# Performance work log

Measured on AMD Instinct MI355X. Metric: run time of the kernel, lower is better.

Reference implementation:

```python
import jax, jax.numpy as jnp
import numpy as np
import math

L, Bt, IN, H = 512, 128, 512, 60


def setup_inputs() -> dict:
    key = jax.random.key(0)
    k1, k2, k3 = jax.random.split(key, 3)
    inp = jax.random.normal(k1, (L, Bt, IN), dtype=jnp.float32)
    W = jax.random.normal(k2, (H, IN), dtype=jnp.float32) / np.sqrt(IN)
    b = jnp.zeros((H,), dtype=jnp.float32)
    alphabet = jax.random.uniform(k3, (H, 3), dtype=jnp.float32, minval=-math.pi, maxval=math.pi)
    bond_lengths = jnp.array([132.868, 145.801, 152.326], dtype=jnp.float32)
    bond_angles = jnp.array([2.028, 2.124, 1.941], dtype=jnp.float32)
    return {"inp": inp, "W": W, "b": b, "alphabet": alphabet,
            "bond_lengths": bond_lengths, "bond_angles": bond_angles}


def reference(inp, W, b, alphabet, bond_lengths, bond_angles):
    Lr, Bb = inp.shape[0], inp.shape[1]
    # mixture over alphabet of torsion angles
    x = jax.nn.softmax(inp @ W.T + b, axis=2)                 # (L, B, H)
    phi = jnp.arctan2(x @ jnp.sin(alphabet), x @ jnp.cos(alphabet))  # (L, B, 3)
    # per residue i the loop consumes phi[i].T -> bond index is fastest axis
    phi_f = phi.transpose(0, 2, 1).reshape(Lr * 3, Bb)        # (3L, B)
    r = jnp.tile(bond_lengths, Lr)[:, None]                   # (3L, 1)
    th = jnp.tile(bond_angles, Lr)[:, None]                   # (3L, 1)
    # SRF coordinates of every new atom
    c_tilde = jnp.stack([
        (r * jnp.cos(th)) * jnp.ones_like(phi_f),
        r * jnp.cos(phi_f) * jnp.sin(th),
        r * jnp.sin(phi_f) * jnp.sin(th),
    ], axis=-1)                                               # (3L, B, 3)

    e = jnp.eye(3, dtype=inp.dtype)
    carry0 = (jnp.broadcast_to(e[0], (Bb, 3)),
              jnp.broadcast_to(e[1], (Bb, 3)),
              jnp.broadcast_to(e[2], (Bb, 3)))

    def step(carry, ct):
        A, Bp, C = carry                                      # each (B, 3)
        BC = C - Bp
        bc = BC / jnp.linalg.norm(BC, axis=1, keepdims=True)
        AB = Bp - A
        Nv = jnp.cross(AB, bc)
        n = Nv / jnp.linalg.norm(Nv, axis=1, keepdims=True)
        # D = C + R @ c_tilde, R columns = [bc, n x bc, n]
        D = C + bc * ct[:, 0:1] + jnp.cross(n, bc) * ct[:, 1:2] + n * ct[:, 2:3]
        return (Bp, C, D), D

    _, coords = jax.lax.scan(step, carry0, c_tilde)           # (3L, B, 3)
    return coords
```

## Files before the change

kernel.cpp:

```cpp
#include <hip/hip_runtime.h>
#include <math.h>

#define LSEQ  512
#define BT    128
#define INF   512
#define HH    60
#define NSTEP 1536
#define CH2   6

#define MTILE 64
#define KSTG  128
#define BROW  136

typedef __attribute__((ext_vector_type(8))) short bf16x8;
typedef __attribute__((ext_vector_type(4))) float floatx4;

__device__ __forceinline__ unsigned cvt_pk_bf16(float lo, float hi) {
  unsigned r;
  asm("v_cvt_pk_bf16_f32 %0, %1, %2" : "=v"(r) : "v"(lo), "v"(hi));
  return r;
}
__device__ __forceinline__ void split_pair(float a0, float a1,
                                           unsigned& hw, unsigned& lw) {
  hw = cvt_pk_bf16(a0, a1);
  float h0 = __uint_as_float(hw << 16);
  float h1 = __uint_as_float(hw & 0xFFFF0000u);
  lw = cvt_pk_bf16(a0 - h0, a1 - h1);
}


#define ISSUE_A(BUF, KB) \
  { _Pragma("unroll") \
    for (int ks_ = 0; ks_ < 4; ++ks_) { \
      BUF[2*ks_]   = *(const float4*)(ap0 + (KB) + ks_*32); \
      BUF[2*ks_+1] = *(const float4*)(ap0 + (KB) + ks_*32 + 4); } }

#define STAGE_W(KB) \
  { _Pragma("unroll") \
    for (int i_ = 0; i_ < 8; ++i_) { \
      const int chunk_ = i_ * 256 + tid; \
      const int r_  = chunk_ >> 5; \
      const int j4_ = (chunk_ & 31) * 4; \
      float4 wv_ = make_float4(0.f, 0.f, 0.f, 0.f); \
      if (r_ < HH) wv_ = *(const float4*)(W + (size_t)r_ * INF + (KB) + j4_); \
      unsigned h01_, l01_, h23_, l23_; \
      split_pair(wv_.x, wv_.y, h01_, l01_); \
      split_pair(wv_.z, wv_.w, h23_, l23_); \
      *(uint2*)&BhL[r_ * BROW + j4_] = make_uint2(h01_, h23_); \
      *(uint2*)&BlL[r_ * BROW + j4_] = make_uint2(l01_, l23_); } }

#define DO_STEPS(BUF) \
  { _Pragma("unroll") \
    for (int ks_ = 0; ks_ < 4; ++ks_) { \
      const int kl_ = ks_ * 32; \
      float4 x_ = BUF[2*ks_], y_ = BUF[2*ks_+1]; \
      uint4 uh_, ul_; \
      split_pair(x_.x, x_.y, uh_.x, ul_.x); \
      split_pair(x_.z, x_.w, uh_.y, ul_.y); \
      split_pair(y_.x, y_.y, uh_.z, ul_.z); \
      split_pair(y_.z, y_.w, uh_.w, ul_.w); \
      bf16x8 Ah_ = __builtin_bit_cast(bf16x8, uh_); \
      bf16x8 Al_ = __builtin_bit_cast(bf16x8, ul_); \
      _Pragma("unroll") \
      for (int nt_ = 0; nt_ < 4; ++nt_) { \
        const int boff_ = (nt_ * 16 + c) * BROW + kl_ + quad * 8; \
        bf16x8 Bh_ = *(const bf16x8*)&BhL[boff_]; \
        bf16x8 Bl_ = *(const bf16x8*)&BlL[boff_]; \
        acc[nt_] = __builtin_amdgcn_mfma_f32_16x16x32_bf16(Ah_, Bh_, acc[nt_], 0, 0, 0); \
        acc[nt_] = __builtin_amdgcn_mfma_f32_16x16x32_bf16(Ah_, Bl_, acc[nt_], 0, 0, 0); \
        acc[nt_] = __builtin_amdgcn_mfma_f32_16x16x32_bf16(Al_, Bh_, acc[nt_], 0, 0, 0); } } }

__global__ __launch_bounds__(256, 3) void k_phi(
    const float* __restrict__ inp, const float* __restrict__ W,
    const float* __restrict__ bias, const float* __restrict__ alphabet,
    float* __restrict__ phi_out) {
  __shared__ unsigned short BhL[64 * BROW];
  __shared__ unsigned short BlL[64 * BROW];
  __shared__ float sS[HH * 3], sC[HH * 3], sBias[64];

  const int tid  = threadIdx.x;
  const int lane = tid & 63;
  const int wid  = tid >> 6;
  const int c    = lane & 15;
  const int quad = lane >> 4;
  const int row0 = blockIdx.x * MTILE;

  if (tid < HH * 3) { float a = alphabet[tid]; sS[tid] = __sinf(a); sC[tid] = __cosf(a); }
  if (tid >= 192 && tid < 256) { int n = tid - 192; sBias[n] = (n < HH) ? bias[n] : 0.f; }

  floatx4 acc[4];
#pragma unroll
  for (int nt = 0; nt < 4; ++nt) acc[nt] = (floatx4){0.f, 0.f, 0.f, 0.f};

  const float* ap0 = inp + (size_t)(row0 + wid * 16 + c) * INF + quad * 8;

  float4 A0[8], A1[8];

  ISSUE_A(A0, 0);
  STAGE_W(0);
  __syncthreads();
  ISSUE_A(A1, KSTG);
  DO_STEPS(A0);
  __syncthreads();
  STAGE_W(KSTG);
  __syncthreads();
  ISSUE_A(A0, 2 * KSTG);
  DO_STEPS(A1);
  __syncthreads();
  STAGE_W(2 * KSTG);
  __syncthreads();
  ISSUE_A(A1, 3 * KSTG);
  DO_STEPS(A0);
  __syncthreads();
  STAGE_W(3 * KSTG);
  __syncthreads();
  DO_STEPS(A1);

#pragma unroll
  for (int reg = 0; reg < 4; ++reg) {
    float lg[4];  bool val[4];
#pragma unroll
    for (int nt = 0; nt < 4; ++nt) {
      const int n = nt * 16 + c;
      val[nt] = (n < HH);
      lg[nt] = acc[nt][reg] + sBias[n];
    }
    float m = -1e30f;
#pragma unroll
    for (int nt = 0; nt < 4; ++nt) if (val[nt]) m = fmaxf(m, lg[nt]);
#pragma unroll
    for (int d = 1; d < 16; d <<= 1) m = fmaxf(m, __shfl_xor(m, d, 64));

    float s0=0.f,c0=0.f,s1=0.f,c1=0.f,s2=0.f,c2=0.f;
#pragma unroll
    for (int nt = 0; nt < 4; ++nt) {
      const int n = nt * 16 + c;
      float e = val[nt] ? __expf(lg[nt] - m) : 0.f;
      s0 = fmaf(e, sS[n*3+0], s0);  c0 = fmaf(e, sC[n*3+0], c0);
      s1 = fmaf(e, sS[n*3+1], s1);  c1 = fmaf(e, sC[n*3+1], c1);
      s2 = fmaf(e, sS[n*3+2], s2);  c2 = fmaf(e, sC[n*3+2], c2);
    }
#pragma unroll
    for (int d = 1; d < 16; d <<= 1) {
      s0 += __shfl_xor(s0, d, 64);  c0 += __shfl_xor(c0, d, 64);
      s1 += __shfl_xor(s1, d, 64);  c1 += __shfl_xor(c1, d, 64);
      s2 += __shfl_xor(s2, d, 64);  c2 += __shfl_xor(c2, d, 64);
    }
    if (c == 0) {
      const int row = row0 + wid * 16 + quad * 4 + reg;
      const int l  = row >> 7;
      const int bb = row & 127;
      float* pp = phi_out + (size_t)bb * NSTEP + 3 * l;
      pp[0] = atan2f(s0, c0);
      pp[1] = atan2f(s1, c1);
      pp[2] = atan2f(s2, c2);
    }
  }
}

struct Xf { float r[9]; float p[3]; };

__device__ __forceinline__ Xf compose(const Xf& A, const Xf& B) {
  Xf o;
#pragma unroll
  for (int i = 0; i < 3; ++i) {
#pragma unroll
    for (int j = 0; j < 3; ++j) {
      o.r[i*3+j] = fmaf(A.r[i*3+0], B.r[0+j],
                   fmaf(A.r[i*3+1], B.r[3+j],
                        A.r[i*3+2] * B.r[6+j]));
    }
    o.p[i] = fmaf(A.r[i*3+0], B.p[0],
             fmaf(A.r[i*3+1], B.p[1],
             fmaf(A.r[i*3+2], B.p[2], A.p[i])));
  }
  return o;
}

__device__ __forceinline__ Xf make_T(float phi, float st, float ct, float r) {
  float sp = __sinf(phi), cp = __cosf(phi);
  Xf T;
  T.r[0] = ct;      T.r[1] = -st;     T.r[2] = 0.f;
  T.r[3] = cp * st; T.r[4] = ct * cp; T.r[5] = -sp;
  T.r[6] = sp * st; T.r[7] = ct * sp; T.r[8] = cp;
  T.p[0] = r * ct;  T.p[1] = r * T.r[3]; T.p[2] = r * T.r[6];
  return T;
}

__device__ __forceinline__ void set_identity(Xf& X) {
  X.r[0]=1.f; X.r[1]=0.f; X.r[2]=0.f;
  X.r[3]=0.f; X.r[4]=1.f; X.r[5]=0.f;
  X.r[6]=0.f; X.r[7]=0.f; X.r[8]=1.f;
  X.p[0]=0.f; X.p[1]=0.f; X.p[2]=0.f;
}

__global__ __launch_bounds__(256) void k_scan(
    const float* __restrict__ phi, const float* __restrict__ bl,
    const float* __restrict__ ba, float* __restrict__ out) {
  __shared__ Xf wt[4];

  const int b = blockIdx.x;
  const int t = threadIdx.x & 63;
  const int w = threadIdx.x >> 6;
  const int g = threadIdx.x;

  float st[3], ct[3], rr[3];
#pragma unroll
  for (int j = 0; j < 3; ++j) {
    float a = ba[j];
    st[j] = __sinf(a); ct[j] = __cosf(a); rr[j] = bl[j];
  }

  float f[CH2];
  const float2* ph2 = (const float2*)(phi + (size_t)b * NSTEP + g * CH2);
#pragma unroll
  for (int q = 0; q < CH2/2; ++q) {
    float2 v = ph2[q];
    f[2*q+0] = v.x; f[2*q+1] = v.y;
  }

  Xf Q = make_T(f[0], st[0], ct[0], rr[0]);
#pragma unroll
  for (int s = 1; s < CH2; ++s)
    Q = compose(Q, make_T(f[s], st[s%3], ct[s%3], rr[s%3]));

#pragma unroll
  for (int d = 1; d < 64; d <<= 1) {
    Xf O;
#pragma unroll
    for (int q = 0; q < 9; ++q) O.r[q] = __shfl_up(Q.r[q], d, 64);
#pragma unroll
    for (int q = 0; q < 3; ++q) O.p[q] = __shfl_up(Q.p[q], d, 64);
    if (t < d) set_identity(O);
    Q = compose(O, Q);
  }

  if (t == 63) wt[w] = Q;
  __syncthreads();

  Xf E;
#pragma unroll
  for (int q = 0; q < 9; ++q) E.r[q] = __shfl_up(Q.r[q], 1, 64);
#pragma unroll
  for (int q = 0; q < 3; ++q) E.p[q] = __shfl_up(Q.p[q], 1, 64);
  if (t == 0) set_identity(E);

  Xf S0;
  S0.r[0] = 0.f;                  S0.r[1] = 0.816496580927726f;   S0.r[2] = 0.5773502691896258f;
  S0.r[3] = -0.7071067811865475f; S0.r[4] = -0.4082482904638631f; S0.r[5] = 0.5773502691896258f;
  S0.r[6] = 0.7071067811865475f;  S0.r[7] = -0.4082482904638631f; S0.r[8] = 0.5773502691896258f;
  S0.p[0] = 0.f; S0.p[1] = 0.f; S0.p[2] = 1.f;

  Xf SP = S0;
#pragma unroll
  for (int i = 0; i < 3; ++i)
    if (i < w) SP = compose(SP, wt[i]);

  Xf cur = compose(SP, E);

  float* op = out + (size_t)(g * CH2) * (BT * 3) + b * 3;
#pragma unroll
  for (int s = 0; s < CH2; ++s) {
    cur = compose(cur, make_T(f[s], st[s%3], ct[s%3], rr[s%3]));
    op[(size_t)s * (BT*3) + 0] = cur.p[0];
    op[(size_t)s * (BT*3) + 1] = cur.p[1];
    op[(size_t)s * (BT*3) + 2] = cur.p[2];
  }
}

extern "C" void kernel_launch(void* const* d_in, const int* in_sizes, int n_in,
                              void* d_out, int out_size, void* d_ws, size_t ws_size,
                              hipStream_t stream) {
  const float* inp      = (const float*)d_in[0];
  const float* W        = (const float*)d_in[1];
  const float* bias     = (const float*)d_in[2];
  const float* alphabet = (const float*)d_in[3];
  const float* bl       = (const float*)d_in[4];
  const float* ba       = (const float*)d_in[5];
  float* out = (float*)d_out;

  float* phi = (float*)d_ws;

  k_phi<<<dim3((LSEQ*BT)/MTILE), dim3(256), 0, stream>>>(inp, W, bias, alphabet, phi);
  k_scan<<<dim3(BT), dim3(256), 0, stream>>>(phi, bl, ba, out);
}
```

Baseline: 228.3 us.

## Hand-schedule global loads with inline asm and explicit vmcnt waits in GEMM pipeline

Replaces compiler-generated loads of the input and W tiles with inline-asm global_load_dwordx4, using SGPR bases and precomputed VGPR offsets. The W loads are issued into registers together with the next A tile, and explicit s_waitcnt vmcnt counts let the W split start while A loads are still in flight. __syncthreads is replaced by a barrier that waits only on lgkmcnt. The aim is to overlap W fetch latency with other memory traffic and cut address arithmetic. The cost is relying on exact in-order vmcnt accounting and on the clamped offset for the padding rows of the last W chunk.

```diff
diff --git a/kernel.cpp b/kernel.cpp
--- a/kernel.cpp
+++ b/kernel.cpp
@@ -28,24 +28,43 @@
   lw = cvt_pk_bf16(a0 - h0, a1 - h1);
 }
 
+#define GLOAD(dst, ptr, voff) \
+  asm volatile("global_load_dwordx4 %0, %1, %2" \
+               : "=v"(dst) : "v"(voff), "s"(ptr))
+
+#define WAIT_VM(n) \
+  do { asm volatile("s_waitcnt vmcnt(" #n ")" ::: "memory"); \
+       __builtin_amdgcn_sched_barrier(0); } while (0)
+
+#define BARRIER() \
+  do { asm volatile("s_waitcnt lgkmcnt(0)" ::: "memory"); \
+       __builtin_amdgcn_s_barrier(); \
+       asm volatile("" ::: "memory"); } while (0)
+
 
 #define ISSUE_A(BUF, KB) \
   { _Pragma("unroll") \
     for (int ks_ = 0; ks_ < 4; ++ks_) { \
-      BUF[2*ks_]   = *(const float4*)(ap0 + (KB) + ks_*32); \
-      BUF[2*ks_+1] = *(const float4*)(ap0 + (KB) + ks_*32 + 4); } }
-
-#define STAGE_W(KB) \
+      GLOAD(BUF[2*ks_],   aBase + (KB) + ks_*32,     voffA); \
+      GLOAD(BUF[2*ks_+1], aBase + (KB) + ks_*32 + 4, voffA); } }
+
+#define ISSUE_W(KB) \
+  { _Pragma("unroll") \
+    for (int i_ = 0; i_ < 7; ++i_) \
+      GLOAD(Wb[i_], W + (KB) + i_*4096, voffW); \
+    GLOAD(Wb[7], W + (KB) + 7*4096, voffWc); }
+
+#define SPLIT_W() \
   { _Pragma("unroll") \
     for (int i_ = 0; i_ < 8; ++i_) { \
       const int chunk_ = i_ * 256 + tid; \
       const int r_  = chunk_ >> 5; \
       const int j4_ = (chunk_ & 31) * 4; \
-      float4 wv_ = make_float4(0.f, 0.f, 0.f, 0.f); \
-      if (r_ < HH) wv_ = *(const float4*)(W + (size_t)r_ * INF + (KB) + j4_); \
+      floatx4 wv_ = Wb[i_]; \
+      if (i_ == 7 && tid >= 128) wv_ = (floatx4){0.f, 0.f, 0.f, 0.f}; \
       unsigned h01_, l01_, h23_, l23_; \
-      split_pair(wv_.x, wv_.y, h01_, l01_); \
-      split_pair(wv_.z, wv_.w, h23_, l23_); \
+      split_pair(wv_[0], wv_[1], h01_, l01_); \
+      split_pair(wv_[2], wv_[3], h23_, l23_); \
       *(uint2*)&BhL[r_ * BROW + j4_] = make_uint2(h01_, h23_); \
       *(uint2*)&BlL[r_ * BROW + j4_] = make_uint2(l01_, l23_); } }
 
@@ -53,12 +72,12 @@
   { _Pragma("unroll") \
     for (int ks_ = 0; ks_ < 4; ++ks_) { \
       const int kl_ = ks_ * 32; \
-      float4 x_ = BUF[2*ks_], y_ = BUF[2*ks_+1]; \
+      floatx4 x_ = BUF[2*ks_], y_ = BUF[2*ks_+1]; \
       uint4 uh_, ul_; \
-      split_pair(x_.x, x_.y, uh_.x, ul_.x); \
-      split_pair(x_.z, x_.w, uh_.y, ul_.y); \
-      split_pair(y_.x, y_.y, uh_.z, ul_.z); \
-      split_pair(y_.z, y_.w, uh_.w, ul_.w); \
+      split_pair(x_[0], x_[1], uh_.x, ul_.x); \
+      split_pair(x_[2], x_[3], uh_.y, ul_.y); \
+      split_pair(y_[0], y_[1], uh_.z, ul_.z); \
+      split_pair(y_[2], y_[3], uh_.w, ul_.w); \
       bf16x8 Ah_ = __builtin_bit_cast(bf16x8, uh_); \
       bf16x8 Al_ = __builtin_bit_cast(bf16x8, ul_); \
       _Pragma("unroll") \
@@ -92,28 +111,42 @@
 #pragma unroll
   for (int nt = 0; nt < 4; ++nt) acc[nt] = (floatx4){0.f, 0.f, 0.f, 0.f};
 
-  const float* ap0 = inp + (size_t)(row0 + wid * 16 + c) * INF + quad * 8;
-
-  float4 A0[8], A1[8];
+  const float* aBase = inp + (size_t)row0 * INF;
+  const unsigned voffA  = ((unsigned)(wid * 16 + c) * INF + quad * 8) * 4u;
+  const unsigned voffW  = ((unsigned)(tid >> 5) * INF + (tid & 31) * 4) * 4u;
+  const unsigned voffWc = (tid < 128) ? voffW : 0u;
+
+  floatx4 A0[8], A1[8], Wb[8];
 
   ISSUE_A(A0, 0);
-  STAGE_W(0);
-  __syncthreads();
+  ISSUE_W(0);
   ISSUE_A(A1, KSTG);
+  WAIT_VM(8);
+  SPLIT_W();
+  BARRIER();
   DO_STEPS(A0);
-  __syncthreads();
-  STAGE_W(KSTG);
-  __syncthreads();
+  BARRIER();
+
+  ISSUE_W(KSTG);
   ISSUE_A(A0, 2 * KSTG);
+  WAIT_VM(8);
+  SPLIT_W();
+  BARRIER();
   DO_STEPS(A1);
-  __syncthreads();
-  STAGE_W(2 * KSTG);
-  __syncthreads();
+  BARRIER();
+
+  ISSUE_W(2 * KSTG);
   ISSUE_A(A1, 3 * KSTG);
+  WAIT_VM(8);
+  SPLIT_W();
+  BARRIER();
   DO_STEPS(A0);
-  __syncthreads();
-  STAGE_W(3 * KSTG);
-  __syncthreads();
+  BARRIER();
+
+  ISSUE_W(3 * KSTG);
+  WAIT_VM(0);
+  SPLIT_W();
+  BARRIER();
   DO_STEPS(A1);
 
 #pragma unroll
```

Measured after the change: 212.8 us. 6.8% less time.
